# Kernel tuning notes

Measured on AMD Instinct MI355X. Metric: run time of the kernel, lower is better.

## Reference

```python
import jax, jax.numpy as jnp
import numpy as np

LAT_MIN, LAT_MAX = -90.0, 90.0
LON_MIN, LON_MAX = 0.0, 360.0
N_LEVELS = 4
N_FEAT = 2
FINEST = 0.25
BASE = 1.0
LAT_SHAPE, LON_SHAPE = 720, 1440
GEODESIC_WEIGHT = True
TABLE = (LAT_SHAPE + 1) * (LON_SHAPE + 1)  # 1038961
# corner offsets in the torch BOX_OFFSETS order: (0,0),(0,1),(1,0),(1,1)
OFFS = np.array([[0, 0], [0, 1], [1, 0], [1, 1]], dtype=np.int32)


def setup_inputs() -> dict:
    key = jax.random.key(0)
    k1, k2 = jax.random.split(key)
    B = 2_000_000
    u = jax.random.uniform(k1, (B, 2), dtype=jnp.float32)
    # lat in [-90, 90), lon in [0, 360)
    x = jnp.stack([u[:, 0] * 180.0 - 90.0, u[:, 1] * 360.0], axis=1)
    embeddings = jax.random.uniform(k2, (N_LEVELS, TABLE, N_FEAT),
                                    minval=-1e-4, maxval=1e-4, dtype=jnp.float32)
    return {"x": x, "embeddings": embeddings}


def _geodesic(lat1, lon1, lat2, lon2):
    r = jnp.pi / 180.0
    rl1, rl2 = lat1 * r, lat2 * r
    dlat = (lat2 - lat1) * r
    dlon = (lon2 - lon1) * r
    a = jnp.sin(dlat / 2) ** 2 + jnp.cos(rl1) * jnp.cos(rl2) * jnp.sin(dlon / 2) ** 2
    return 2.0 * jnp.arctan2(jnp.sqrt(a), jnp.sqrt(1.0 - a))


def reference(x, embeddings):
    box_min = jnp.array([LAT_MIN - FINEST, LON_MIN - FINEST], dtype=x.dtype)
    box_max = jnp.array([LAT_MAX + FINEST, LON_MAX + FINEST], dtype=x.dtype)
    xc = jnp.clip(x, box_min, box_max)  # clamped coords used for grid indexing
    offs = jnp.asarray(OFFS)
    outs = []
    for i in range(N_LEVELS):
        gs = BASE * (2.0 ** i)  # grid size (same for lat and lon)
        bl = jnp.floor((xc - box_min) / gs).astype(jnp.int32)  # [B,2] bottom-left idx
        gmin = bl.astype(x.dtype) * gs + box_min                # [B,2]
        gmax = gmin + gs
        width = int(np.floor(LON_SHAPE / gs))
        # 4 corner flat indices: lat_idx * width + lon_idx -> [B,4]
        idx = (bl[:, 0:1] + offs[None, :, 0]) * width + (bl[:, 1:2] + offs[None, :, 1])
        e = embeddings[i][idx]  # gather: [B,4,F]
        if GEODESIC_WEIGHT:
            wlat = _geodesic(gmin[:, 0], gmin[:, 1], x[:, 0], gmin[:, 1]) / \
                   _geodesic(gmin[:, 0], gmin[:, 1], gmax[:, 0], gmin[:, 1])
            wlon = _geodesic(gmin[:, 0], x[:, 1], gmin[:, 0], gmax[:, 1]) / \
                   _geodesic(gmin[:, 0], gmin[:, 1], gmin[:, 0], gmax[:, 1])
        else:
            w = (x - gmin) / (gmax - gmin)
            wlat, wlon = w[:, 0], w[:, 1]
        # bilinear blend (corner order: 0=(0,0) 1=(0,1) 2=(1,0) 3=(1,1))
        c0 = e[:, 0] * (1 - wlat[:, None]) + e[:, 2] * wlat[:, None]
        c1 = e[:, 1] * (1 - wlat[:, None]) + e[:, 3] * wlat[:, None]
        outs.append(c0 * (1 - wlon[:, None]) + c1 * wlon[:, None])
    return jnp.concatenate(outs, axis=-1)  # [B, N_LEVELS*N_FEAT]
```

## Files before the change

kernel.cpp:

```cpp
#include <hip/hip_runtime.h>
#include <hip/hip_fp16.h>

#define NT 256

constexpr int TABLE_SZ = 721 * 1441;

constexpr int QLAT = 181, QLON = 361;
constexpr int NCELLS = QLAT * QLON;

constexpr int LUT_OFF0 = 0, LUT_OFF1 = 181, LUT_OFF2 = 272, LUT_OFF3 = 318;
constexpr int LUT_N = 341;

typedef float v4f __attribute__((ext_vector_type(4)));
typedef float v2f __attribute__((ext_vector_type(2)));

__device__ __constant__ float c_s2_tab[4] = {0.008726535498f, 0.017452406437f,
                                             0.034899496703f, 0.069756473744f};

__global__ __launch_bounds__(256)
void build_superquad(const float* __restrict__ emb, uint4* __restrict__ sq)
{
    int c = blockIdx.x * 256 + threadIdx.x;
    if (c >= NCELLS) return;
    int la = c / QLON, lo = c - la * QLON;
    const float2* embv = (const float2*)emb;
    #pragma unroll
    for (int i = 0; i < 4; ++i) {
        const int width = 1440 >> i;
        const int ra = la >> i, co = lo >> i;
        const float2* t = embv + (size_t)i * TABLE_SZ;
        float2 e0 = t[ra * width + co];
        float2 e1 = t[ra * width + co + 1];
        float2 e2 = t[(ra + 1) * width + co];
        float2 e3 = t[(ra + 1) * width + co + 1];
        union { uint4 u; __half2 h[4]; } pk;
        pk.h[0] = __floats2half2_rn(e0.x, e0.y);
        pk.h[1] = __floats2half2_rn(e1.x, e1.y);
        pk.h[2] = __floats2half2_rn(e2.x, e2.y);
        pk.h[3] = __floats2half2_rn(e3.x, e3.y);
        sq[(size_t)c * 4 + i] = pk.u;
    }
}

template <bool USE_SQ>
__global__ __launch_bounds__(NT)
void ngp_interp_kernel(const float* __restrict__ x,
                       const float* __restrict__ emb,
                       const uint4* __restrict__ sq,
                       float* __restrict__ out,
                       int B)
{
    const float r = 0.017453292519943295f;
    const float bmin_lat = -90.25f;
    const float bmin_lon = -0.25f;

    __shared__ float2 lut[LUT_N];
    for (int t = threadIdx.x; t < LUT_N; t += NT) {
        int lvl, row;
        if (t < LUT_OFF1)      { lvl = 0; row = t; }
        else if (t < LUT_OFF2) { lvl = 1; row = t - LUT_OFF1; }
        else if (t < LUT_OFF3) { lvl = 2; row = t - LUT_OFF2; }
        else                   { lvl = 3; row = t - LUT_OFF3; }
        const float gs = (float)(1 << lvl);
        const float gmin_lat = (float)row * gs + bmin_lat;
        const float ca = fabsf(__cosf(gmin_lat * r));
        const float z2 = ca * c_s2_tab[lvl];
        const float n2 = z2 + z2 * z2 * z2 * (1.0f / 6.0f);
        lut[t] = make_float2(ca, __builtin_amdgcn_rcpf(n2));
    }
    __syncthreads();

    const int p = blockIdx.x * NT + threadIdx.x;
    if (p >= B) return;

    const v2f xp = __builtin_nontemporal_load(reinterpret_cast<const v2f*>(x) + p);
    const float xlat = xp.x;
    const float xlon = xp.y;

    const float bmax_lat = 90.25f, bmax_lon = 360.25f;
    const float xc_lat = fminf(fmaxf(xlat, bmin_lat), bmax_lat);
    const float xc_lon = fminf(fmaxf(xlon, bmin_lon), bmax_lon);

    const float v_lat = xc_lat - bmin_lat;
    const float v_lon = xc_lon - bmin_lon;

    const int cell0 = (int)floorf(v_lat) * QLON + (int)floorf(v_lon);
    const uint4* cellp = sq + (size_t)cell0 * 4;

    const int lut_off[4] = {LUT_OFF0, LUT_OFF1, LUT_OFF2, LUT_OFF3};

    float o[8];

    #pragma unroll
    for (int i = 0; i < 4; ++i) {
        const float gs     = (float)(1 << i);
        const float inv_gs = 1.0f / gs;
        const int   width  = 1440 >> i;

        const float blat_f = floorf(v_lat * inv_gs);
        const float blon_f = floorf(v_lon * inv_gs);
        const float gmin_lat = blat_f * gs + bmin_lat;
        const float gmin_lon = blon_f * gs + bmin_lon;
        const float gmax_lon = gmin_lon + gs;
        const int bl_lat = (int)blat_f;

        v2f E0, E1, E2, E3;
        if (USE_SQ) {
            union { uint4 u; __half2 h[4]; } pk;
            pk.u = cellp[i];
            float2 f0 = __half22float2(pk.h[0]);
            float2 f1 = __half22float2(pk.h[1]);
            float2 f2 = __half22float2(pk.h[2]);
            float2 f3 = __half22float2(pk.h[3]);
            E0 = (v2f){f0.x, f0.y}; E1 = (v2f){f1.x, f1.y};
            E2 = (v2f){f2.x, f2.y}; E3 = (v2f){f3.x, f3.y};
        } else {
            const int bl_lon = (int)blon_f;
            const int idx00 = bl_lat * width + bl_lon;
            const float* base0 = emb + ((size_t)i * TABLE_SZ + (size_t)idx00) * 2;
            const float* base1 = base0 + (size_t)width * 2;
            v4f eA, eB;
            __builtin_memcpy(&eA, base0, 16);
            __builtin_memcpy(&eB, base1, 16);
            E0 = (v2f){eA.x, eA.y}; E1 = (v2f){eA.z, eA.w};
            E2 = (v2f){eB.x, eB.y}; E3 = (v2f){eB.z, eB.w};
        }

        const float wlat = (xlat - gmin_lat) * inv_gs;

        const float2 cl = lut[lut_off[i] + bl_lat];
        const float h1 = (gmax_lon - xlon) * r * 0.5f;
        const float s1 = h1 - h1 * h1 * h1 * (1.0f / 6.0f);
        const float z1 = cl.x * s1;
        const float n1 = z1 + z1 * z1 * z1 * (1.0f / 6.0f);
        const float wlon = n1 * cl.y;

        const v2f wa = {wlat, wlat};
        const v2f wo = {wlon, wlon};
        const v2f c0 = E0 + (E2 - E0) * wa;
        const v2f c1 = E1 + (E3 - E1) * wa;
        const v2f res = c0 + (c1 - c0) * wo;
        o[2*i]   = res.x;
        o[2*i+1] = res.y;
    }

    v4f* op = reinterpret_cast<v4f*>(out + (size_t)p * 8);
    v4f lo = {o[0], o[1], o[2], o[3]};
    v4f hi = {o[4], o[5], o[6], o[7]};
    __builtin_nontemporal_store(lo, op);
    __builtin_nontemporal_store(hi, op + 1);
}

extern "C" void kernel_launch(void* const* d_in, const int* in_sizes, int n_in,
                              void* d_out, int out_size, void* d_ws, size_t ws_size,
                              hipStream_t stream)
{
    const float* x   = (const float*)d_in[0];
    const float* emb = (const float*)d_in[1];
    float* out = (float*)d_out;
    const int B = in_sizes[0] / 2;
    const int grid = (B + NT - 1) / NT;

    const size_t sq_bytes = (size_t)NCELLS * 64;
    if (ws_size >= sq_bytes) {
        uint4* sq = (uint4*)d_ws;
        build_superquad<<<(NCELLS + 255) / 256, 256, 0, stream>>>(emb, sq);
        ngp_interp_kernel<true><<<grid, NT, 0, stream>>>(x, emb, sq, out, B);
    } else {
        ngp_interp_kernel<false><<<grid, NT, 0, stream>>>(x, emb, nullptr, out, B);
    }
}
```

Baseline: 123.8 us.

## Replace per-fine-cell superquad with per-level packed corner tables

Result: slower. 128.5 us (+3.8%).

```diff
diff --git a/kernel.cpp b/kernel.cpp
--- a/kernel.cpp
+++ b/kernel.cpp
@@ -5,8 +5,13 @@
 
 constexpr int TABLE_SZ = 721 * 1441;
 
-constexpr int QLAT = 181, QLON = 361;
-constexpr int NCELLS = QLAT * QLON;
+constexpr int H0 = 181, W0 = 361;
+constexpr int H1 = 91,  W1 = 181;
+constexpr int H2 = 46,  W2 = 91;
+constexpr int H3 = 23,  W3 = 46;
+constexpr int N0 = H0 * W0, N1 = H1 * W1, N2 = H2 * W2, N3 = H3 * W3;
+constexpr int TOFF0 = 0, TOFF1 = N0, TOFF2 = N0 + N1, TOFF3 = N0 + N1 + N2;
+constexpr int NTOT = N0 + N1 + N2 + N3;
 
 constexpr int LUT_OFF0 = 0, LUT_OFF1 = 181, LUT_OFF2 = 272, LUT_OFF3 = 318;
 constexpr int LUT_N = 341;
@@ -18,35 +23,37 @@
                                              0.034899496703f, 0.069756473744f};
 
 __global__ __launch_bounds__(256)
-void build_superquad(const float* __restrict__ emb, uint4* __restrict__ sq)
+void build_tables(const float* __restrict__ emb, uint4* __restrict__ tab)
 {
-    int c = blockIdx.x * 256 + threadIdx.x;
-    if (c >= NCELLS) return;
-    int la = c / QLON, lo = c - la * QLON;
-    const float2* embv = (const float2*)emb;
-    #pragma unroll
-    for (int i = 0; i < 4; ++i) {
-        const int width = 1440 >> i;
-        const int ra = la >> i, co = lo >> i;
-        const float2* t = embv + (size_t)i * TABLE_SZ;
-        float2 e0 = t[ra * width + co];
-        float2 e1 = t[ra * width + co + 1];
-        float2 e2 = t[(ra + 1) * width + co];
-        float2 e3 = t[(ra + 1) * width + co + 1];
-        union { uint4 u; __half2 h[4]; } pk;
-        pk.h[0] = __floats2half2_rn(e0.x, e0.y);
-        pk.h[1] = __floats2half2_rn(e1.x, e1.y);
-        pk.h[2] = __floats2half2_rn(e2.x, e2.y);
-        pk.h[3] = __floats2half2_rn(e3.x, e3.y);
-        sq[(size_t)c * 4 + i] = pk.u;
-    }
+    const int t = blockIdx.x * 256 + threadIdx.x;
+    if (t >= NTOT) return;
+
+    int lvl, ra, co;
+    if (t < TOFF1)      { lvl = 0; const int i = t;         ra = i / W0; co = i - ra * W0; }
+    else if (t < TOFF2) { lvl = 1; const int i = t - TOFF1; ra = i / W1; co = i - ra * W1; }
+    else if (t < TOFF3) { lvl = 2; const int i = t - TOFF2; ra = i / W2; co = i - ra * W2; }
+    else                { lvl = 3; const int i = t - TOFF3; ra = i / W3; co = i - ra * W3; }
+
+    const int width = 1440 >> lvl;
+    const float2* tb = (const float2*)emb + (size_t)lvl * TABLE_SZ;
+    const float2 e0 = tb[ra * width + co];
+    const float2 e1 = tb[ra * width + co + 1];
+    const float2 e2 = tb[(ra + 1) * width + co];
+    const float2 e3 = tb[(ra + 1) * width + co + 1];
+
+    union { uint4 u; __half2 h[4]; } pk;
+    pk.h[0] = __floats2half2_rn(e0.x, e0.y);
+    pk.h[1] = __floats2half2_rn(e1.x, e1.y);
+    pk.h[2] = __floats2half2_rn(e2.x, e2.y);
+    pk.h[3] = __floats2half2_rn(e3.x, e3.y);
+    tab[t] = pk.u;
 }
 
 template <bool USE_SQ>
 __global__ __launch_bounds__(NT)
 void ngp_interp_kernel(const float* __restrict__ x,
                        const float* __restrict__ emb,
-                       const uint4* __restrict__ sq,
+                       const uint4* __restrict__ tab,
                        float* __restrict__ out,
                        int B)
 {
@@ -84,8 +91,21 @@
     const float v_lat = xc_lat - bmin_lat;
     const float v_lon = xc_lon - bmin_lon;
 
-    const int cell0 = (int)floorf(v_lat) * QLON + (int)floorf(v_lon);
-    const uint4* cellp = sq + (size_t)cell0 * 4;
+    float blatf[4], blonf[4];
+    #pragma unroll
+    for (int i = 0; i < 4; ++i) {
+        const float inv_gs = 1.0f / (float)(1 << i);
+        blatf[i] = floorf(v_lat * inv_gs);
+        blonf[i] = floorf(v_lon * inv_gs);
+    }
+
+    uint4 g[4];
+    if (USE_SQ) {
+        g[0] = tab[TOFF0 + (int)blatf[0] * W0 + (int)blonf[0]];
+        g[1] = tab[TOFF1 + (int)blatf[1] * W1 + (int)blonf[1]];
+        g[2] = tab[TOFF2 + (int)blatf[2] * W2 + (int)blonf[2]];
+        g[3] = tab[TOFF3 + (int)blatf[3] * W3 + (int)blonf[3]];
+    }
 
     const int lut_off[4] = {LUT_OFF0, LUT_OFF1, LUT_OFF2, LUT_OFF3};
 
@@ -97,17 +117,15 @@
         const float inv_gs = 1.0f / gs;
         const int   width  = 1440 >> i;
 
-        const float blat_f = floorf(v_lat * inv_gs);
-        const float blon_f = floorf(v_lon * inv_gs);
-        const float gmin_lat = blat_f * gs + bmin_lat;
-        const float gmin_lon = blon_f * gs + bmin_lon;
+        const float gmin_lat = blatf[i] * gs + bmin_lat;
+        const float gmin_lon = blonf[i] * gs + bmin_lon;
         const float gmax_lon = gmin_lon + gs;
-        const int bl_lat = (int)blat_f;
+        const int bl_lat = (int)blatf[i];
 
         v2f E0, E1, E2, E3;
         if (USE_SQ) {
             union { uint4 u; __half2 h[4]; } pk;
-            pk.u = cellp[i];
+            pk.u = g[i];
             float2 f0 = __half22float2(pk.h[0]);
             float2 f1 = __half22float2(pk.h[1]);
             float2 f2 = __half22float2(pk.h[2]);
@@ -115,7 +133,7 @@
             E0 = (v2f){f0.x, f0.y}; E1 = (v2f){f1.x, f1.y};
             E2 = (v2f){f2.x, f2.y}; E3 = (v2f){f3.x, f3.y};
         } else {
-            const int bl_lon = (int)blon_f;
+            const int bl_lon = (int)blonf[i];
             const int idx00 = bl_lat * width + bl_lon;
             const float* base0 = emb + ((size_t)i * TABLE_SZ + (size_t)idx00) * 2;
             const float* base1 = base0 + (size_t)width * 2;
@@ -161,11 +179,11 @@
     const int B = in_sizes[0] / 2;
     const int grid = (B + NT - 1) / NT;
 
-    const size_t sq_bytes = (size_t)NCELLS * 64;
-    if (ws_size >= sq_bytes) {
-        uint4* sq = (uint4*)d_ws;
-        build_superquad<<<(NCELLS + 255) / 256, 256, 0, stream>>>(emb, sq);
-        ngp_interp_kernel<true><<<grid, NT, 0, stream>>>(x, emb, sq, out, B);
+    const size_t tab_bytes = (size_t)NTOT * sizeof(uint4);
+    if (ws_size >= tab_bytes) {
+        uint4* tab = (uint4*)d_ws;
+        build_tables<<<(NTOT + 255) / 256, 256, 0, stream>>>(emb, tab);
+        ngp_interp_kernel<true><<<grid, NT, 0, stream>>>(x, emb, tab, out, B);
     } else {
         ngp_interp_kernel<false><<<grid, NT, 0, stream>>>(x, emb, nullptr, out, B);
     }
```
